# Kernel optimization log

Measured on AMD Instinct MI355X. Metric: run time of the kernel, lower is better.

Reference implementation:

```python
import jax, jax.numpy as jnp
import numpy as np

RES = 512
NUM_COMP = 64
INIT_SCALE = 0.1
N_PTS = 1048576


def setup_inputs() -> dict:
    key = jax.random.key(0)
    k1, k2 = jax.random.split(key)
    # points in [-1, 1] as the module expects
    in_tensor = jax.random.uniform(k1, (N_PTS, 3), dtype=jnp.float32, minval=-1.0, maxval=1.0)
    plane_coef = INIT_SCALE * jax.random.normal(k2, (3, NUM_COMP, RES, RES), dtype=jnp.float32)
    return {"in_tensor": in_tensor, "plane_coef": plane_coef}


def _sample_plane(coef, xy):
    """Bilinear grid_sample, align_corners=True, padding_mode='border'.

    coef: (C, R, R) feature plane; xy: (N, 2) coords in [-1, 1], xy[:,0]->W, xy[:,1]->H.
    Returns (C, N).
    """
    C, R, _ = coef.shape
    # unnormalize (align_corners=True), then border-clamp the coordinate itself
    fx = jnp.clip((xy[:, 0] + 1.0) * 0.5 * (R - 1), 0.0, R - 1)
    fy = jnp.clip((xy[:, 1] + 1.0) * 0.5 * (R - 1), 0.0, R - 1)
    x0 = jnp.floor(fx)
    y0 = jnp.floor(fy)
    wx = fx - x0
    wy = fy - y0
    x0i = x0.astype(jnp.int32)
    y0i = y0.astype(jnp.int32)
    x1i = jnp.minimum(x0i + 1, R - 1)
    y1i = jnp.minimum(y0i + 1, R - 1)
    flat = coef.reshape(C, R * R)  # gather via flat indices: idx = y*R + x

    def g(yi, xi):
        return flat[:, yi * R + xi]  # (C, N)

    return (g(y0i, x0i) * ((1.0 - wx) * (1.0 - wy))
            + g(y0i, x1i) * (wx * (1.0 - wy))
            + g(y1i, x0i) * ((1.0 - wx) * wy)
            + g(y1i, x1i) * (wx * wy))


def reference(in_tensor, plane_coef):
    orig_shape = in_tensor.shape
    pts = in_tensor.reshape(-1, 3)
    # projections onto the xy, xz, yz planes, matching torch order
    coords = jnp.stack([pts[:, jnp.array([0, 1])],
                        pts[:, jnp.array([0, 2])],
                        pts[:, jnp.array([1, 2])]], axis=0)  # (3, N, 2)
    feats = jax.vmap(_sample_plane)(plane_coef, coords)  # (3, C, N)
    out = feats.sum(0).T  # mode == 'sum' -> (N, C)
    return out.reshape(*orig_shape[:-1], -1)
```

## Files before the change

### kernel.cpp

```cpp
#include <hip/hip_runtime.h>

#define RES   512
#define NCH   64
#define SP    (RES * RES)

#define NBITS 5
#define NSIDE (1 << NBITS)
#define NBINS (1 << (3 * NBITS))

#define TRBLK 6144

typedef float v4f __attribute__((ext_vector_type(4)));

__device__ __forceinline__ v4f nt_load4(const float* p)
{
    return __builtin_nontemporal_load((const v4f*)p);
}
__device__ __forceinline__ void nt_store4(float* p, v4f v)
{
    __builtin_nontemporal_store(v, (v4f*)p);
}

__device__ __forceinline__ unsigned part1by2(unsigned v)
{
    v &= 0x3FF;
    v = (v | (v << 16)) & 0x030000FF;
    v = (v | (v <<  8)) & 0x0300F00F;
    v = (v | (v <<  4)) & 0x030C30C3;
    v = (v | (v <<  2)) & 0x09249249;
    return v;
}

__device__ __forceinline__ unsigned bin_of(float x, float y, float z)
{
    int ix = (int)((x + 1.0f) * 0.5f * (float)NSIDE);
    int iy = (int)((y + 1.0f) * 0.5f * (float)NSIDE);
    int iz = (int)((z + 1.0f) * 0.5f * (float)NSIDE);
    ix = min(max(ix, 0), NSIDE - 1);
    iy = min(max(iy, 0), NSIDE - 1);
    iz = min(max(iz, 0), NSIDE - 1);
    return part1by2((unsigned)ix) | (part1by2((unsigned)iy) << 1)
         | (part1by2((unsigned)iz) << 2);
}

__global__ __launch_bounds__(256) void transpose_hist(
    const float* __restrict__ in, float* __restrict__ out,
    const float* __restrict__ pts, unsigned* __restrict__ hist, int npts)
{
    __shared__ float tile[64][129];

    int b = blockIdx.x;
    if (b >= TRBLK) {
        int i = (b - TRBLK) * 256 + threadIdx.x;
        if (i < npts) {
            float x = pts[3 * (size_t)i + 0];
            float y = pts[3 * (size_t)i + 1];
            float z = pts[3 * (size_t)i + 2];
            atomicAdd(&hist[bin_of(x, y, z)], 1u);
        }
        return;
    }

    int plane = b >> 11;
    int s0    = (b & 2047) << 7;
    const float* src = in  + (size_t)plane * NCH * SP;
    float*       dst = out + (size_t)plane * SP  * NCH;

    int tid = threadIdx.x;
    int r   = tid >> 4;
    int c4  = (tid & 15) << 2;

    v4f vv[8];
    #pragma unroll
    for (int it = 0; it < 8; ++it) {
        int ch = r + (it & 3) * 16;
        int sp = ((it >> 2) << 6) + c4;
        vv[it] = nt_load4(src + (size_t)ch * SP + s0 + sp);
    }
    #pragma unroll
    for (int it = 0; it < 8; ++it) {
        int ch = r + (it & 3) * 16;
        int sp = ((it >> 2) << 6) + c4;
        tile[ch][sp + 0] = vv[it][0];
        tile[ch][sp + 1] = vv[it][1];
        tile[ch][sp + 2] = vv[it][2];
        tile[ch][sp + 3] = vv[it][3];
    }
    __syncthreads();
    #pragma unroll
    for (int it = 0; it < 8; ++it) {
        int s = r + (it & 3) * 16 + ((it >> 2) << 6);
        v4f v;
        v[0] = tile[c4 + 0][s];
        v[1] = tile[c4 + 1][s];
        v[2] = tile[c4 + 2][s];
        v[3] = tile[c4 + 3][s];
        *(v4f*)(dst + (size_t)(s0 + s) * NCH + c4) = v;
    }
}

__global__ __launch_bounds__(1024) void scan_kernel(
    const unsigned* __restrict__ hist, unsigned* __restrict__ offs)
{
    __shared__ unsigned partial[1024];
    int t = threadIdx.x;
    unsigned base = (unsigned)t * 32;
    unsigned local[32];
    unsigned s = 0;
    #pragma unroll
    for (int k = 0; k < 32; ++k) { local[k] = s; s += hist[base + k]; }
    partial[t] = s;
    __syncthreads();
    for (int d = 1; d < 1024; d <<= 1) {
        unsigned v = (t >= d) ? partial[t - d] : 0u;
        __syncthreads();
        partial[t] += v;
        __syncthreads();
    }
    unsigned chunk_excl = (t == 0) ? 0u : partial[t - 1];
    #pragma unroll
    for (int k = 0; k < 32; ++k) offs[base + k] = chunk_excl + local[k];
}

__global__ __launch_bounds__(256) void scatter_kernel(
    const float* __restrict__ pts, unsigned* __restrict__ offs,
    float* __restrict__ spts4, int npts)
{
    int i = blockIdx.x * 256 + threadIdx.x;
    if (i >= npts) return;
    float x = pts[3 * (size_t)i + 0];
    float y = pts[3 * (size_t)i + 1];
    float z = pts[3 * (size_t)i + 2];
    unsigned pos = atomicAdd(&offs[bin_of(x, y, z)], 1u);
    v4f v;
    v[0] = x; v[1] = y; v[2] = z; v[3] = __uint_as_float((unsigned)i);
    *(v4f*)(spts4 + 4 * (size_t)pos) = v;
}

__global__ __launch_bounds__(256) void gather_sorted(
    const float* __restrict__ spts4,
    const float* __restrict__ tp, float* __restrict__ out,
    int npts, int nblk)
{
    int cpx = nblk >> 3;
    int b   = blockIdx.x;
    int swz = (b & 7) * cpx + (b >> 3);
    int t   = swz * 256 + threadIdx.x;
    int j   = t >> 4;
    if (j >= npts) return;
    int cg  = (t & 15) << 2;

    v4f s = *(const v4f*)(spts4 + 4 * (size_t)j);
    float px = s[0], py = s[1], pz = s[2];
    unsigned idx = __float_as_uint(s[3]);

    float us[3] = {px, px, py};
    float vs[3] = {py, pz, pz};

    v4f acc = {0.f, 0.f, 0.f, 0.f};

    #pragma unroll
    for (int pl = 0; pl < 3; ++pl) {
        float fx = fminf(fmaxf((us[pl] + 1.0f) * 0.5f * 511.0f, 0.0f), 511.0f);
        float fy = fminf(fmaxf((vs[pl] + 1.0f) * 0.5f * 511.0f, 0.0f), 511.0f);
        float x0f = floorf(fx), y0f = floorf(fy);
        int   x0  = (int)x0f,  y0  = (int)y0f;
        float wx  = fx - x0f,  wy  = fy - y0f;
        int   x1  = min(x0 + 1, RES - 1);
        int   y1  = min(y0 + 1, RES - 1);

        const float* base = tp + (size_t)pl * SP * NCH;
        v4f v00 = *(const v4f*)(base + ((size_t)(y0 * RES + x0) * NCH) + cg);
        v4f v01 = *(const v4f*)(base + ((size_t)(y0 * RES + x1) * NCH) + cg);
        v4f v10 = *(const v4f*)(base + ((size_t)(y1 * RES + x0) * NCH) + cg);
        v4f v11 = *(const v4f*)(base + ((size_t)(y1 * RES + x1) * NCH) + cg);

        float w00 = (1.0f - wx) * (1.0f - wy);
        float w01 = wx * (1.0f - wy);
        float w10 = (1.0f - wx) * wy;
        float w11 = wx * wy;

        acc += w00 * v00 + w01 * v01 + w10 * v10 + w11 * v11;
    }

    nt_store4(out + (size_t)idx * NCH + cg, acc);
}

__global__ __launch_bounds__(256) void gather_tp(
    const float* __restrict__ pts,
    const float* __restrict__ tp,
    float* __restrict__ out, int npts)
{
    int t  = blockIdx.x * 256 + threadIdx.x;
    int pt = t >> 4;
    if (pt >= npts) return;
    int cg = (t & 15) << 2;

    float px = pts[3 * (size_t)pt + 0];
    float py = pts[3 * (size_t)pt + 1];
    float pz = pts[3 * (size_t)pt + 2];

    float us[3] = {px, px, py};
    float vs[3] = {py, pz, pz};

    v4f acc = {0.f, 0.f, 0.f, 0.f};

    #pragma unroll
    for (int pl = 0; pl < 3; ++pl) {
        float fx = fminf(fmaxf((us[pl] + 1.0f) * 0.5f * 511.0f, 0.0f), 511.0f);
        float fy = fminf(fmaxf((vs[pl] + 1.0f) * 0.5f * 511.0f, 0.0f), 511.0f);
        float x0f = floorf(fx), y0f = floorf(fy);
        int   x0  = (int)x0f,  y0  = (int)y0f;
        float wx  = fx - x0f,  wy  = fy - y0f;
        int   x1  = min(x0 + 1, RES - 1);
        int   y1  = min(y0 + 1, RES - 1);

        const float* base = tp + (size_t)pl * SP * NCH;
        v4f v00 = *(const v4f*)(base + ((size_t)(y0 * RES + x0) * NCH) + cg);
        v4f v01 = *(const v4f*)(base + ((size_t)(y0 * RES + x1) * NCH) + cg);
        v4f v10 = *(const v4f*)(base + ((size_t)(y1 * RES + x0) * NCH) + cg);
        v4f v11 = *(const v4f*)(base + ((size_t)(y1 * RES + x1) * NCH) + cg);

        float w00 = (1.0f - wx) * (1.0f - wy);
        float w01 = wx * (1.0f - wy);
        float w10 = (1.0f - wx) * wy;
        float w11 = wx * wy;

        acc += w00 * v00 + w01 * v01 + w10 * v10 + w11 * v11;
    }

    *(v4f*)(out + (size_t)pt * NCH + cg) = acc;
}

__global__ __launch_bounds__(256) void gather_direct(
    const float* __restrict__ pts,
    const float* __restrict__ planes,
    float* __restrict__ out, int npts)
{
    long t = (long)blockIdx.x * 256 + threadIdx.x;
    int pt = (int)(t >> 6);
    if (pt >= npts) return;
    int ch = (int)(t & 63);

    float px = pts[3 * (size_t)pt + 0];
    float py = pts[3 * (size_t)pt + 1];
    float pz = pts[3 * (size_t)pt + 2];
    float us[3] = {px, px, py};
    float vs[3] = {py, pz, pz};

    float acc = 0.0f;
    #pragma unroll
    for (int pl = 0; pl < 3; ++pl) {
        float fx = fminf(fmaxf((us[pl] + 1.0f) * 0.5f * 511.0f, 0.0f), 511.0f);
        float fy = fminf(fmaxf((vs[pl] + 1.0f) * 0.5f * 511.0f, 0.0f), 511.0f);
        float x0f = floorf(fx), y0f = floorf(fy);
        int   x0  = (int)x0f,  y0  = (int)y0f;
        float wx  = fx - x0f,  wy  = fy - y0f;
        int   x1  = min(x0 + 1, RES - 1);
        int   y1  = min(y0 + 1, RES - 1);

        const float* base = planes + (size_t)pl * NCH * SP + (size_t)ch * SP;
        float v00 = base[y0 * RES + x0];
        float v01 = base[y0 * RES + x1];
        float v10 = base[y1 * RES + x0];
        float v11 = base[y1 * RES + x1];

        acc += v00 * ((1.0f - wx) * (1.0f - wy))
             + v01 * (wx * (1.0f - wy))
             + v10 * ((1.0f - wx) * wy)
             + v11 * (wx * wy);
    }
    out[(size_t)pt * NCH + ch] = acc;
}

extern "C" void kernel_launch(void* const* d_in, const int* in_sizes, int n_in,
                              void* d_out, int out_size, void* d_ws, size_t ws_size,
                              hipStream_t stream)
{
    (void)n_in; (void)out_size;
    const float* pts    = (const float*)d_in[0];
    const float* planes = (const float*)d_in[1];
    float*       out    = (float*)d_out;
    int npts = in_sizes[0] / 3;

    size_t sz_tp     = (size_t)3 * NCH * SP * sizeof(float);
    size_t off_spts  = sz_tp;
    size_t sz_spts   = (size_t)npts * 4 * sizeof(float);
    size_t off_hist  = off_spts + sz_spts;
    size_t off_offs  = off_hist + (size_t)NBINS * sizeof(unsigned);
    size_t need_sort = off_offs + (size_t)NBINS * sizeof(unsigned);

    int nptblk = (npts + 255) / 256;

    if (ws_size >= need_sort) {
        float*    tp   = (float*)d_ws;
        float*    sp4  = (float*)((char*)d_ws + off_spts);
        unsigned* hist = (unsigned*)((char*)d_ws + off_hist);
        unsigned* offs = (unsigned*)((char*)d_ws + off_offs);

        hipMemsetAsync(hist, 0, (size_t)NBINS * sizeof(unsigned), stream);
        transpose_hist<<<TRBLK + nptblk, 256, 0, stream>>>(
            planes, tp, pts, hist, npts);
        scan_kernel<<<1, 1024, 0, stream>>>(hist, offs);
        scatter_kernel<<<nptblk, 256, 0, stream>>>(pts, offs, sp4, npts);

        long nthr = (long)npts * 16;
        int  nblk = (int)((nthr + 255) / 256);
        nblk = (nblk + 7) & ~7;
        gather_sorted<<<nblk, 256, 0, stream>>>(sp4, tp, out, npts, nblk);
    } else if (ws_size >= sz_tp) {
        transpose_hist<<<TRBLK, 256, 0, stream>>>(
            planes, (float*)d_ws, nullptr, nullptr, 0);
        long nthr = (long)npts * 16;
        gather_tp<<<(int)((nthr + 255) / 256), 256, 0, stream>>>(
            pts, (const float*)d_ws, out, npts);
    } else {
        long nthr = (long)npts * 64;
        gather_direct<<<(int)((nthr + 255) / 256), 256, 0, stream>>>(
            pts, planes, out, npts);
    }
}
```

Baseline: 665.5 us.

## Move plane transpose into scatter kernel and double-buffer transpose tiles

The plane transpose used to be fused with the histogram pass. It now runs in the same launch as the scatter pass, and the histogram gets its own small kernel, so the short single-block scan no longer stalls the large transpose. The transpose blocks now handle 256 spatial positions through a 32-channel shared tile, issuing the loads for the second channel half before storing the first half. This overlaps global loads with shared-memory work at the cost of more registers and extra barriers. The sorted-point read in the gather is also made nontemporal.

After: 692.6 us. 1.04x slower.

```diff
diff --git a/kernel.cpp b/kernel.cpp
--- a/kernel.cpp
+++ b/kernel.cpp
@@ -8,7 +8,7 @@
 #define NSIDE (1 << NBITS)
 #define NBINS (1 << (3 * NBITS))
 
-#define TRBLK 6144
+#define TRBLK 3072
 
 typedef float v4f __attribute__((ext_vector_type(4)));
 
@@ -43,60 +43,15 @@
          | (part1by2((unsigned)iz) << 2);
 }
 
-__global__ __launch_bounds__(256) void transpose_hist(
-    const float* __restrict__ in, float* __restrict__ out,
+__global__ __launch_bounds__(256) void hist_kernel(
     const float* __restrict__ pts, unsigned* __restrict__ hist, int npts)
 {
-    __shared__ float tile[64][129];
-
-    int b = blockIdx.x;
-    if (b >= TRBLK) {
-        int i = (b - TRBLK) * 256 + threadIdx.x;
-        if (i < npts) {
-            float x = pts[3 * (size_t)i + 0];
-            float y = pts[3 * (size_t)i + 1];
-            float z = pts[3 * (size_t)i + 2];
-            atomicAdd(&hist[bin_of(x, y, z)], 1u);
-        }
-        return;
-    }
-
-    int plane = b >> 11;
-    int s0    = (b & 2047) << 7;
-    const float* src = in  + (size_t)plane * NCH * SP;
-    float*       dst = out + (size_t)plane * SP  * NCH;
-
-    int tid = threadIdx.x;
-    int r   = tid >> 4;
-    int c4  = (tid & 15) << 2;
-
-    v4f vv[8];
-    #pragma unroll
-    for (int it = 0; it < 8; ++it) {
-        int ch = r + (it & 3) * 16;
-        int sp = ((it >> 2) << 6) + c4;
-        vv[it] = nt_load4(src + (size_t)ch * SP + s0 + sp);
-    }
-    #pragma unroll
-    for (int it = 0; it < 8; ++it) {
-        int ch = r + (it & 3) * 16;
-        int sp = ((it >> 2) << 6) + c4;
-        tile[ch][sp + 0] = vv[it][0];
-        tile[ch][sp + 1] = vv[it][1];
-        tile[ch][sp + 2] = vv[it][2];
-        tile[ch][sp + 3] = vv[it][3];
-    }
-    __syncthreads();
-    #pragma unroll
-    for (int it = 0; it < 8; ++it) {
-        int s = r + (it & 3) * 16 + ((it >> 2) << 6);
-        v4f v;
-        v[0] = tile[c4 + 0][s];
-        v[1] = tile[c4 + 1][s];
-        v[2] = tile[c4 + 2][s];
-        v[3] = tile[c4 + 3][s];
-        *(v4f*)(dst + (size_t)(s0 + s) * NCH + c4) = v;
-    }
+    int i = blockIdx.x * 256 + threadIdx.x;
+    if (i >= npts) return;
+    float x = pts[3 * (size_t)i + 0];
+    float y = pts[3 * (size_t)i + 1];
+    float z = pts[3 * (size_t)i + 2];
+    atomicAdd(&hist[bin_of(x, y, z)], 1u);
 }
 
 __global__ __launch_bounds__(1024) void scan_kernel(
@@ -122,19 +77,90 @@
     for (int k = 0; k < 32; ++k) offs[base + k] = chunk_excl + local[k];
 }
 
-__global__ __launch_bounds__(256) void scatter_kernel(
+__global__ __launch_bounds__(256) void transpose_scatter(
+    const float* __restrict__ in, float* __restrict__ out,
     const float* __restrict__ pts, unsigned* __restrict__ offs,
     float* __restrict__ spts4, int npts)
 {
-    int i = blockIdx.x * 256 + threadIdx.x;
-    if (i >= npts) return;
-    float x = pts[3 * (size_t)i + 0];
-    float y = pts[3 * (size_t)i + 1];
-    float z = pts[3 * (size_t)i + 2];
-    unsigned pos = atomicAdd(&offs[bin_of(x, y, z)], 1u);
-    v4f v;
-    v[0] = x; v[1] = y; v[2] = z; v[3] = __uint_as_float((unsigned)i);
-    *(v4f*)(spts4 + 4 * (size_t)pos) = v;
+    __shared__ float tile[32][257];
+
+    int b = blockIdx.x;
+    if (b >= TRBLK) {
+        int i = (b - TRBLK) * 256 + threadIdx.x;
+        if (i < npts) {
+            float x = pts[3 * (size_t)i + 0];
+            float y = pts[3 * (size_t)i + 1];
+            float z = pts[3 * (size_t)i + 2];
+            unsigned pos = atomicAdd(&offs[bin_of(x, y, z)], 1u);
+            v4f v;
+            v[0] = x; v[1] = y; v[2] = z; v[3] = __uint_as_float((unsigned)i);
+            *(v4f*)(spts4 + 4 * (size_t)pos) = v;
+        }
+        return;
+    }
+
+    int plane = b >> 10;
+    int s0    = (b & 1023) << 8;
+    const float* src = in  + (size_t)plane * NCH * SP;
+    float*       dst = out + (size_t)plane * SP  * NCH;
+
+    int t   = threadIdx.x;
+    int lch = t >> 3;
+    int lsp = (t & 7) << 2;
+    int sch = (t & 7) << 2;
+    int ssp = t >> 3;
+
+    v4f ra[8], rb[8];
+
+    #pragma unroll
+    for (int i = 0; i < 8; ++i)
+        ra[i] = nt_load4(src + (size_t)lch * SP + s0 + lsp + i * 32);
+    #pragma unroll
+    for (int i = 0; i < 8; ++i) {
+        int sp = lsp + i * 32;
+        tile[lch][sp + 0] = ra[i][0];
+        tile[lch][sp + 1] = ra[i][1];
+        tile[lch][sp + 2] = ra[i][2];
+        tile[lch][sp + 3] = ra[i][3];
+    }
+    __syncthreads();
+
+    #pragma unroll
+    for (int i = 0; i < 8; ++i)
+        rb[i] = nt_load4(src + (size_t)(lch + 32) * SP + s0 + lsp + i * 32);
+
+    #pragma unroll
+    for (int j = 0; j < 8; ++j) {
+        int s = ssp + j * 32;
+        v4f v;
+        v[0] = tile[sch + 0][s];
+        v[1] = tile[sch + 1][s];
+        v[2] = tile[sch + 2][s];
+        v[3] = tile[sch + 3][s];
+        *(v4f*)(dst + (size_t)(s0 + s) * NCH + sch) = v;
+    }
+    __syncthreads();
+
+    #pragma unroll
+    for (int i = 0; i < 8; ++i) {
+        int sp = lsp + i * 32;
+        tile[lch][sp + 0] = rb[i][0];
+        tile[lch][sp + 1] = rb[i][1];
+        tile[lch][sp + 2] = rb[i][2];
+        tile[lch][sp + 3] = rb[i][3];
+    }
+    __syncthreads();
+
+    #pragma unroll
+    for (int j = 0; j < 8; ++j) {
+        int s = ssp + j * 32;
+        v4f v;
+        v[0] = tile[sch + 0][s];
+        v[1] = tile[sch + 1][s];
+        v[2] = tile[sch + 2][s];
+        v[3] = tile[sch + 3][s];
+        *(v4f*)(dst + (size_t)(s0 + s) * NCH + 32 + sch) = v;
+    }
 }
 
 __global__ __launch_bounds__(256) void gather_sorted(
@@ -150,7 +176,7 @@
     if (j >= npts) return;
     int cg  = (t & 15) << 2;
 
-    v4f s = *(const v4f*)(spts4 + 4 * (size_t)j);
+    v4f s = nt_load4(spts4 + 4 * (size_t)j);
     float px = s[0], py = s[1], pz = s[2];
     unsigned idx = __float_as_uint(s[3]);
 
@@ -299,18 +325,18 @@
         unsigned* offs = (unsigned*)((char*)d_ws + off_offs);
 
         hipMemsetAsync(hist, 0, (size_t)NBINS * sizeof(unsigned), stream);
-        transpose_hist<<<TRBLK + nptblk, 256, 0, stream>>>(
-            planes, tp, pts, hist, npts);
+        hist_kernel<<<nptblk, 256, 0, stream>>>(pts, hist, npts);
         scan_kernel<<<1, 1024, 0, stream>>>(hist, offs);
-        scatter_kernel<<<nptblk, 256, 0, stream>>>(pts, offs, sp4, npts);
+        transpose_scatter<<<TRBLK + nptblk, 256, 0, stream>>>(
+            planes, tp, pts, offs, sp4, npts);
 
         long nthr = (long)npts * 16;
         int  nblk = (int)((nthr + 255) / 256);
         nblk = (nblk + 7) & ~7;
         gather_sorted<<<nblk, 256, 0, stream>>>(sp4, tp, out, npts, nblk);
     } else if (ws_size >= sz_tp) {
-        transpose_hist<<<TRBLK, 256, 0, stream>>>(
-            planes, (float*)d_ws, nullptr, nullptr, 0);
+        transpose_scatter<<<TRBLK, 256, 0, stream>>>(
+            planes, (float*)d_ws, nullptr, nullptr, nullptr, 0);
         long nthr = (long)npts * 16;
         gather_tp<<<(int)((nthr + 255) / 256), 256, 0, stream>>>(
             pts, (const float*)d_ws, out, npts);
```
